# Kernel tuning notes

Measured on AMD Instinct MI355X. Metric: run time of the kernel, lower is better.

## Reference

```python
import jax, jax.numpy as jnp
import numpy as np

ORDER = 3  # polynomial filter order


def _sketch_conv(x, A, W, b, coeffs):
    # z = A @ (x W + b); out = sum_d coeffs[d-1] * z**d  (Horner-free power accumulation)
    z = A @ (x @ W + b)            # [N, out_c]
    p = z
    acc = coeffs[0] * z
    for d in range(1, ORDER):      # small fixed loop over polynomial order
        p = p * z
        acc = acc + coeffs[d] * p
    return acc


def setup_inputs() -> dict:
    key = jax.random.key(0)
    ks = jax.random.split(key, 12)
    N, C_IN, C_H, C_OUT = 8192, 128, 64, 40
    nf_mats = jax.random.normal(ks[0], (N, C_IN), dtype=jnp.float32)
    # scale by 1/sqrt(N) so polynomial powers stay O(1)
    conv_mats = jax.random.normal(ks[1], (N, N), dtype=jnp.float32) / np.float32(np.sqrt(N))
    def lin(k, fi, fo):
        kw, kb = jax.random.split(k)
        W = jax.random.normal(kw, (fi, fo), dtype=jnp.float32) / np.float32(np.sqrt(fi))
        b = jax.random.normal(kb, (fo,), dtype=jnp.float32) * np.float32(0.01)
        return W, b
    W1, b1 = lin(ks[2], C_IN, C_H)
    W2, b2 = lin(ks[3], C_H, C_H)
    W3, b3 = lin(ks[4], C_H, C_OUT)
    base = jnp.array([1.0, 0.0, 0.0], dtype=jnp.float32)
    c1 = base + jax.random.normal(ks[5], (ORDER,), dtype=jnp.float32) * 0.05
    c2 = base + jax.random.normal(ks[6], (ORDER,), dtype=jnp.float32) * 0.05
    c3 = base + jax.random.normal(ks[7], (ORDER,), dtype=jnp.float32) * 0.05
    return {"nf_mats": nf_mats, "conv_mats": conv_mats,
            "W1": W1, "b1": b1, "c1": c1,
            "W2": W2, "b2": b2, "c2": c2,
            "W3": W3, "b3": b3, "c3": c3}


def reference(nf_mats, conv_mats, W1, b1, c1, W2, b2, c2, W3, b3, c3):
    # SketchGCN eval-mode forward: batchnorm=False, dropout inactive.
    x = _sketch_conv(nf_mats, conv_mats, W1, b1, c1)      # first layer
    x = x + _sketch_conv(x, conv_mats, W2, b2, c2)        # residual middle layer
    return _sketch_conv(x, conv_mats, W3, b3, c3)         # output layer
```

## Files before the change

### kernel.cpp

```cpp
#include <hip/hip_runtime.h>
#include <stdint.h>

typedef __bf16 bf16x8 __attribute__((ext_vector_type(8)));
typedef float f32x4 __attribute__((ext_vector_type(4)));

using gvoid = const __attribute__((address_space(1))) void;
using lvoid = __attribute__((address_space(3))) void;

__device__ __forceinline__ unsigned short f2bf(float f) {
    union { float f; unsigned u; } x; x.f = f;
    unsigned u = x.u;
    u += 0x7FFFu + ((u >> 16) & 1u);
    return (unsigned short)(u >> 16);
}
__device__ __forceinline__ unsigned pack2(float lo, float hi) {
    return ((unsigned)f2bf(hi) << 16) | (unsigned)f2bf(lo);
}

template <int CIN>
__global__ __launch_bounds__(256) void small_gemm(const float* __restrict__ X,
                                                  const float* __restrict__ W,
                                                  const float* __restrict__ b,
                                                  int cout,
                                                  unsigned short* __restrict__ Yt) {
    __shared__ float Xs[32 * (CIN + 1)];
    __shared__ float Ws[CIN * 64];
    __shared__ float bs[64];
    const int t = threadIdx.x;
    const int i0 = blockIdx.x * 32;

    for (int e = t; e < 32 * CIN; e += 256) {
        int r = e / CIN, c = e % CIN;
        Xs[r * (CIN + 1) + c] = X[(size_t)(i0 + r) * CIN + c];
    }
    for (int e = t; e < CIN * 64; e += 256) {
        int k = e >> 6, j = e & 63;
        Ws[e] = (j < cout) ? W[k * cout + j] : 0.0f;
    }
    if (t < 64) bs[t] = (t < cout) ? b[t] : 0.0f;
    __syncthreads();

    const int i = t & 31;
    const int jg = t >> 5;
    float acc[8];
#pragma unroll
    for (int jj = 0; jj < 8; ++jj) acc[jj] = 0.0f;

    for (int k = 0; k < CIN; ++k) {
        float xv = Xs[i * (CIN + 1) + k];
        const float4* wr = (const float4*)&Ws[k * 64 + jg * 8];
        float4 w0 = wr[0], w1 = wr[1];
        acc[0] += xv * w0.x; acc[1] += xv * w0.y;
        acc[2] += xv * w0.z; acc[3] += xv * w0.w;
        acc[4] += xv * w1.x; acc[5] += xv * w1.y;
        acc[6] += xv * w1.z; acc[7] += xv * w1.w;
    }
#pragma unroll
    for (int jj = 0; jj < 8; ++jj) {
        int j = jg * 8 + jj;
        Yt[(size_t)j * 8192 + i0 + i] = f2bf(acc[jj] + bs[j]);
    }
}

template <int CONV>
__global__ __launch_bounds__(256, CONV ? 3 : 4)
void big_gemm(const float* __restrict__ Afp,
              unsigned short* __restrict__ Ab,
              const unsigned short* __restrict__ Yt,
              float* __restrict__ P) {
    __shared__ unsigned short As[2][64 * 64];
    __shared__ unsigned short Bs[2][64 * 64];
    const int t = threadIdx.x;
    const int lane = t & 63, wid = t >> 6;
    const int lane15 = lane & 15, lane4 = lane >> 4;
    const int wm = wid >> 1, wn = wid & 1;
    const int row0 = blockIdx.x * 64;
    const int kbase = blockIdx.y * 1024;

    f32x4 acc[2][2];
    const f32x4 z4 = {0.f, 0.f, 0.f, 0.f};
#pragma unroll
    for (int m = 0; m < 2; ++m)
#pragma unroll
        for (int n = 0; n < 2; ++n) acc[m][n] = z4;

    float4 ra[2][2];

    auto loadA_regs = [&](int kt) {
#pragma unroll
        for (int ii = 0; ii < 2; ++ii) {
            int p = ii * 256 + t;
            int r = p >> 3, cl = p & 7;
            const float* gp = Afp + (size_t)(row0 + r) * 8192 + kt + cl * 8;
            ra[ii][0] = *(const float4*)gp;
            ra[ii][1] = *(const float4*)(gp + 4);
        }
    };
    auto writeA = [&](int nb, int kt) {
#pragma unroll
        for (int ii = 0; ii < 2; ++ii) {
            int p = ii * 256 + t;
            int r = p >> 3, cl = p & 7;
            uint4 ch;
            ch.x = pack2(ra[ii][0].x, ra[ii][0].y);
            ch.y = pack2(ra[ii][0].z, ra[ii][0].w);
            ch.z = pack2(ra[ii][1].x, ra[ii][1].y);
            ch.w = pack2(ra[ii][1].z, ra[ii][1].w);
            *(uint4*)&As[nb][((r << 3) | (cl ^ (r & 7))) << 3] = ch;
            *(uint4*)&Ab[(size_t)(row0 + r) * 8192 + kt + cl * 8] = ch;
        }
    };
    auto stageA = [&](int nb, int kt) {
#pragma unroll
        for (int ii = 0; ii < 2; ++ii) {
            int p = ii * 256 + wid * 64 + lane;
            int r = p >> 3;
            int c = (p & 7) ^ (r & 7);
            const unsigned short* gp = Ab + (size_t)(row0 + r) * 8192 + (kt + c * 8);
            unsigned short* lp = &As[nb][(ii * 256 + wid * 64) * 8];
            __builtin_amdgcn_global_load_lds((gvoid*)gp, (lvoid*)lp, 16, 0, 0);
        }
    };
    auto stageB = [&](int nb, int kt) {
#pragma unroll
        for (int ii = 0; ii < 2; ++ii) {
            int q = ii * 256 + wid * 64 + lane;
            int n = q >> 3;
            int c = (q & 7) ^ (n & 7);
            const unsigned short* gp = Yt + (size_t)n * 8192 + (kt + c * 8);
            unsigned short* lp = &Bs[nb][(ii * 256 + wid * 64) * 8];
            __builtin_amdgcn_global_load_lds((gvoid*)gp, (lvoid*)lp, 16, 0, 0);
        }
    };

    if (CONV) {
        loadA_regs(kbase);
        stageB(0, kbase);
        writeA(0, kbase);
    } else {
        stageA(0, kbase);
        stageB(0, kbase);
    }
    __syncthreads();

    int buf = 0;
    const int NIT = 16;
    for (int tt = 0; tt < NIT; ++tt) {
        const bool pre = (tt + 1 < NIT);
        const int kt1 = kbase + (tt + 1) * 64;
        if (pre) {
            if (CONV) {
                loadA_regs(kt1);
                stageB(buf ^ 1, kt1);
            } else {
                stageA(buf ^ 1, kt1);
                stageB(buf ^ 1, kt1);
            }
        }
#pragma unroll
        for (int ks = 0; ks < 2; ++ks) {
            bf16x8 af[2], bfr[2];
#pragma unroll
            for (int m = 0; m < 2; ++m) {
                int r = wm * 32 + m * 16 + lane15;
                int c = ks * 4 + lane4;
                af[m] = *(const bf16x8*)&As[buf][((r << 3) | (c ^ (r & 7))) << 3];
            }
#pragma unroll
            for (int n = 0; n < 2; ++n) {
                int rn = wn * 32 + n * 16 + lane15;
                int c = ks * 4 + lane4;
                bfr[n] = *(const bf16x8*)&Bs[buf][((rn << 3) | (c ^ (rn & 7))) << 3];
            }
#pragma unroll
            for (int m = 0; m < 2; ++m)
#pragma unroll
                for (int n = 0; n < 2; ++n)
                    acc[m][n] = __builtin_amdgcn_mfma_f32_16x16x32_bf16(
                        af[m], bfr[n], acc[m][n], 0, 0, 0);
        }
        if (CONV && pre) writeA(buf ^ 1, kt1);
        __syncthreads();
        buf ^= 1;
    }

    float* Po = P + (size_t)blockIdx.y * (8192 * 64);
#pragma unroll
    for (int m = 0; m < 2; ++m) {
        int r = row0 + wm * 32 + m * 16 + lane4 * 4;
#pragma unroll
        for (int n = 0; n < 2; ++n) {
            int cc = wn * 32 + n * 16 + lane15;
#pragma unroll
            for (int q = 0; q < 4; ++q)
                Po[(size_t)(r + q) * 64 + cc] = acc[m][n][q];
        }
    }
}

template <int MODE>
__global__ __launch_bounds__(256) void fused_reduce(const float* __restrict__ P,
                                                    const float* __restrict__ cf,
                                                    const float* __restrict__ Wn,
                                                    const float* __restrict__ bn,
                                                    int cout,
                                                    float* __restrict__ X1,
                                                    unsigned short* __restrict__ Yt) {
    __shared__ float Xs[64 * 33];
    __shared__ float Ws[64 * 64];
    __shared__ float bs[64];
    const int t = threadIdx.x;
    const int i0 = blockIdx.x * 32;
    const int NT4 = 8192 * 64 / 4;
    const float4* P4 = (const float4*)P;
    float4* X14 = (float4*)X1;

    for (int e = t; e < 64 * 64; e += 256) {
        int k = e >> 6, j = e & 63;
        Ws[e] = (j < cout) ? Wn[k * cout + j] : 0.0f;
    }
    if (t < 64) bs[t] = (t < cout) ? bn[t] : 0.0f;
    const float c0 = cf[0], c1 = cf[1], c2 = cf[2];

#pragma unroll
    for (int s = 0; s < 2; ++s) {
        int e4 = s * 256 + t;
        int i = e4 >> 4, jc = e4 & 15;
        int base4 = (i0 + i) * 16 + jc;
        float4 z = {0.f, 0.f, 0.f, 0.f};
#pragma unroll
        for (int ks = 0; ks < 8; ++ks) {
            float4 p = P4[(size_t)ks * NT4 + base4];
            z.x += p.x; z.y += p.y; z.z += p.z; z.w += p.w;
        }
        float4 v;
        v.x = z.x * (c0 + z.x * (c1 + z.x * c2));
        v.y = z.y * (c0 + z.y * (c1 + z.y * c2));
        v.z = z.z * (c0 + z.z * (c1 + z.z * c2));
        v.w = z.w * (c0 + z.w * (c1 + z.w * c2));
        if (MODE == 0) {
            X14[base4] = v;
        } else {
            float4 xr = X14[base4];
            v.x += xr.x; v.y += xr.y; v.z += xr.z; v.w += xr.w;
        }
        Xs[(jc * 4 + 0) * 33 + i] = v.x;
        Xs[(jc * 4 + 1) * 33 + i] = v.y;
        Xs[(jc * 4 + 2) * 33 + i] = v.z;
        Xs[(jc * 4 + 3) * 33 + i] = v.w;
    }
    __syncthreads();

    const int i = t & 31;
    const int jg = t >> 5;
    float acc[8];
#pragma unroll
    for (int jj = 0; jj < 8; ++jj) acc[jj] = 0.0f;
    for (int k = 0; k < 64; ++k) {
        float xv = Xs[k * 33 + i];
        const float4* wr = (const float4*)&Ws[k * 64 + jg * 8];
        float4 w0 = wr[0], w1 = wr[1];
        acc[0] += xv * w0.x; acc[1] += xv * w0.y;
        acc[2] += xv * w0.z; acc[3] += xv * w0.w;
        acc[4] += xv * w1.x; acc[5] += xv * w1.y;
        acc[6] += xv * w1.z; acc[7] += xv * w1.w;
    }
#pragma unroll
    for (int jj = 0; jj < 8; ++jj) {
        int j = jg * 8 + jj;
        Yt[(size_t)j * 8192 + i0 + i] = f2bf(acc[jj] + bs[j]);
    }
}

__global__ void reduce_out(const float* __restrict__ P, const float* __restrict__ cf,
                           float* __restrict__ out) {
    int e4 = blockIdx.x * 256 + threadIdx.x;
    const int NT4 = 8192 * 64 / 4;
    const float4* P4 = (const float4*)P;
    float4 z = {0.f, 0.f, 0.f, 0.f};
#pragma unroll
    for (int ks = 0; ks < 8; ++ks) {
        float4 p = P4[(size_t)ks * NT4 + e4];
        z.x += p.x; z.y += p.y; z.z += p.z; z.w += p.w;
    }
    float c0 = cf[0], c1 = cf[1], c2 = cf[2];
    float4 v;
    v.x = z.x * (c0 + z.x * (c1 + z.x * c2));
    v.y = z.y * (c0 + z.y * (c1 + z.y * c2));
    v.z = z.z * (c0 + z.z * (c1 + z.z * c2));
    v.w = z.w * (c0 + z.w * (c1 + z.w * c2));
    int i = e4 >> 4, jc = e4 & 15;
    if (jc < 10) ((float4*)out)[i * 10 + jc] = v;
}

extern "C" void kernel_launch(void* const* d_in, const int* in_sizes, int n_in,
                              void* d_out, int out_size, void* d_ws, size_t ws_size,
                              hipStream_t stream) {
    const float* nf   = (const float*)d_in[0];
    const float* Amat = (const float*)d_in[1];
    const float* W1   = (const float*)d_in[2];
    const float* b1   = (const float*)d_in[3];
    const float* c1   = (const float*)d_in[4];
    const float* W2   = (const float*)d_in[5];
    const float* b2   = (const float*)d_in[6];
    const float* c2   = (const float*)d_in[7];
    const float* W3   = (const float*)d_in[8];
    const float* b3   = (const float*)d_in[9];
    const float* c3   = (const float*)d_in[10];
    float* out = (float*)d_out;

    char* ws = (char*)d_ws;
    unsigned short* Abf = (unsigned short*)(ws);
    unsigned short* Yt  = (unsigned short*)(ws + 134217728);
    float* X1           = (float*)(ws + 135266304);
    float* Pp           = (float*)(ws + 137363456);

    small_gemm<128><<<256, 256, 0, stream>>>(nf, W1, b1, 64, Yt);
    big_gemm<1><<<dim3(128, 8), 256, 0, stream>>>(Amat, Abf, Yt, Pp);
    fused_reduce<0><<<256, 256, 0, stream>>>(Pp, c1, W2, b2, 64, X1, Yt);

    big_gemm<0><<<dim3(128, 8), 256, 0, stream>>>(nullptr, Abf, Yt, Pp);
    fused_reduce<1><<<256, 256, 0, stream>>>(Pp, c2, W3, b3, 40, X1, Yt);

    big_gemm<0><<<dim3(128, 8), 256, 0, stream>>>(nullptr, Abf, Yt, Pp);
    reduce_out<<<512, 256, 0, stream>>>(Pp, c3, out);
}
```

Baseline: 223.4 us.

## Load GEMM fragments directly from global into registers, drop LDS staging

The big GEMM kernel no longer stages A and B tiles through shared memory with barriers. Each lane now loads its MFMA fragments straight from global memory into registers, double-buffered in registers across k-steps. In the conversion pass, only one of the two waves sharing a row writes the bf16 A cache. This removes LDS traffic and __syncthreads, but each A and B tile is now fetched by two waves, doubling global/L2 reads, and the row-strided per-lane 16-byte loads coalesce less well.

```diff
diff --git a/kernel.cpp b/kernel.cpp
--- a/kernel.cpp
+++ b/kernel.cpp
@@ -3,9 +3,6 @@
 
 typedef __bf16 bf16x8 __attribute__((ext_vector_type(8)));
 typedef float f32x4 __attribute__((ext_vector_type(4)));
-
-using gvoid = const __attribute__((address_space(1))) void;
-using lvoid = __attribute__((address_space(3))) void;
 
 __device__ __forceinline__ unsigned short f2bf(float f) {
     union { float f; unsigned u; } x; x.f = f;
@@ -16,6 +13,7 @@
 __device__ __forceinline__ unsigned pack2(float lo, float hi) {
     return ((unsigned)f2bf(hi) << 16) | (unsigned)f2bf(lo);
 }
+union U16 { uint4 u; bf16x8 v; };
 
 template <int CIN>
 __global__ __launch_bounds__(256) void small_gemm(const float* __restrict__ X,
@@ -68,14 +66,15 @@
               unsigned short* __restrict__ Ab,
               const unsigned short* __restrict__ Yt,
               float* __restrict__ P) {
-    __shared__ unsigned short As[2][64 * 64];
-    __shared__ unsigned short Bs[2][64 * 64];
     const int t = threadIdx.x;
     const int lane = t & 63, wid = t >> 6;
     const int lane15 = lane & 15, lane4 = lane >> 4;
     const int wm = wid >> 1, wn = wid & 1;
     const int row0 = blockIdx.x * 64;
     const int kbase = blockIdx.y * 1024;
+    const int arow = row0 + wm * 32 + lane15;
+    const int brow = wn * 32 + lane15;
+    const int kc = lane4 * 8;
 
     f32x4 acc[2][2];
     const f32x4 z4 = {0.f, 0.f, 0.f, 0.f};
@@ -84,104 +83,89 @@
 #pragma unroll
         for (int n = 0; n < 2; ++n) acc[m][n] = z4;
 
-    float4 ra[2][2];
-
-    auto loadA_regs = [&](int kt) {
-#pragma unroll
-        for (int ii = 0; ii < 2; ++ii) {
-            int p = ii * 256 + t;
-            int r = p >> 3, cl = p & 7;
-            const float* gp = Afp + (size_t)(row0 + r) * 8192 + kt + cl * 8;
-            ra[ii][0] = *(const float4*)gp;
-            ra[ii][1] = *(const float4*)(gp + 4);
-        }
+    auto loadB = [&](bf16x8 (&bb)[2][2], int kt) {
+#pragma unroll
+        for (int n = 0; n < 2; ++n)
+#pragma unroll
+            for (int ks = 0; ks < 2; ++ks)
+                bb[n][ks] = *(const bf16x8*)(Yt + (size_t)(brow + n * 16) * 8192 +
+                                             kt + ks * 32 + kc);
     };
-    auto writeA = [&](int nb, int kt) {
-#pragma unroll
-        for (int ii = 0; ii < 2; ++ii) {
-            int p = ii * 256 + t;
-            int r = p >> 3, cl = p & 7;
-            uint4 ch;
-            ch.x = pack2(ra[ii][0].x, ra[ii][0].y);
-            ch.y = pack2(ra[ii][0].z, ra[ii][0].w);
-            ch.z = pack2(ra[ii][1].x, ra[ii][1].y);
-            ch.w = pack2(ra[ii][1].z, ra[ii][1].w);
-            *(uint4*)&As[nb][((r << 3) | (cl ^ (r & 7))) << 3] = ch;
-            *(uint4*)&Ab[(size_t)(row0 + r) * 8192 + kt + cl * 8] = ch;
-        }
-    };
-    auto stageA = [&](int nb, int kt) {
-#pragma unroll
-        for (int ii = 0; ii < 2; ++ii) {
-            int p = ii * 256 + wid * 64 + lane;
-            int r = p >> 3;
-            int c = (p & 7) ^ (r & 7);
-            const unsigned short* gp = Ab + (size_t)(row0 + r) * 8192 + (kt + c * 8);
-            unsigned short* lp = &As[nb][(ii * 256 + wid * 64) * 8];
-            __builtin_amdgcn_global_load_lds((gvoid*)gp, (lvoid*)lp, 16, 0, 0);
-        }
-    };
-    auto stageB = [&](int nb, int kt) {
-#pragma unroll
-        for (int ii = 0; ii < 2; ++ii) {
-            int q = ii * 256 + wid * 64 + lane;
-            int n = q >> 3;
-            int c = (q & 7) ^ (n & 7);
-            const unsigned short* gp = Yt + (size_t)n * 8192 + (kt + c * 8);
-            unsigned short* lp = &Bs[nb][(ii * 256 + wid * 64) * 8];
-            __builtin_amdgcn_global_load_lds((gvoid*)gp, (lvoid*)lp, 16, 0, 0);
-        }
-    };
-
-    if (CONV) {
-        loadA_regs(kbase);
-        stageB(0, kbase);
-        writeA(0, kbase);
+
+    if constexpr (CONV) {
+        auto loadT = [&](float4 (&ra)[2][2][2], bf16x8 (&bb)[2][2], int kt) {
+#pragma unroll
+            for (int m = 0; m < 2; ++m)
+#pragma unroll
+                for (int ks = 0; ks < 2; ++ks) {
+                    const float* gp = Afp + (size_t)(arow + m * 16) * 8192 +
+                                      kt + ks * 32 + kc;
+                    ra[m][ks][0] = *(const float4*)gp;
+                    ra[m][ks][1] = *(const float4*)(gp + 4);
+                }
+            loadB(bb, kt);
+        };
+        auto comp = [&](float4 (&ra)[2][2][2], bf16x8 (&bb)[2][2], int kt) {
+#pragma unroll
+            for (int ks = 0; ks < 2; ++ks) {
+                bf16x8 af[2];
+#pragma unroll
+                for (int m = 0; m < 2; ++m) {
+                    U16 u;
+                    u.u.x = pack2(ra[m][ks][0].x, ra[m][ks][0].y);
+                    u.u.y = pack2(ra[m][ks][0].z, ra[m][ks][0].w);
+                    u.u.z = pack2(ra[m][ks][1].x, ra[m][ks][1].y);
+                    u.u.w = pack2(ra[m][ks][1].z, ra[m][ks][1].w);
+                    af[m] = u.v;
+                    if (wn == 0)
+                        *(uint4*)(Ab + (size_t)(arow + m * 16) * 8192 +
+                                  kt + ks * 32 + kc) = u.u;
+                }
+#pragma unroll
+                for (int m = 0; m < 2; ++m)
+#pragma unroll
+                    for (int n = 0; n < 2; ++n)
+                        acc[m][n] = __builtin_amdgcn_mfma_f32_16x16x32_bf16(
+                            af[m], bb[n][ks], acc[m][n], 0, 0, 0);
+            }
+        };
+        float4 raA[2][2][2], raB[2][2][2];
+        bf16x8 bbA[2][2], bbB[2][2];
+        loadT(raA, bbA, kbase);
+        for (int tt = 0; tt < 16; tt += 2) {
+            if (tt + 1 < 16) loadT(raB, bbB, kbase + (tt + 1) * 64);
+            comp(raA, bbA, kbase + tt * 64);
+            if (tt + 2 < 16) loadT(raA, bbA, kbase + (tt + 2) * 64);
+            if (tt + 1 < 16) comp(raB, bbB, kbase + (tt + 1) * 64);
+        }
     } else {
-        stageA(0, kbase);
-        stageB(0, kbase);
-    }
-    __syncthreads();
-
-    int buf = 0;
-    const int NIT = 16;
-    for (int tt = 0; tt < NIT; ++tt) {
-        const bool pre = (tt + 1 < NIT);
-        const int kt1 = kbase + (tt + 1) * 64;
-        if (pre) {
-            if (CONV) {
-                loadA_regs(kt1);
-                stageB(buf ^ 1, kt1);
-            } else {
-                stageA(buf ^ 1, kt1);
-                stageB(buf ^ 1, kt1);
-            }
-        }
-#pragma unroll
-        for (int ks = 0; ks < 2; ++ks) {
-            bf16x8 af[2], bfr[2];
-#pragma unroll
-            for (int m = 0; m < 2; ++m) {
-                int r = wm * 32 + m * 16 + lane15;
-                int c = ks * 4 + lane4;
-                af[m] = *(const bf16x8*)&As[buf][((r << 3) | (c ^ (r & 7))) << 3];
-            }
-#pragma unroll
-            for (int n = 0; n < 2; ++n) {
-                int rn = wn * 32 + n * 16 + lane15;
-                int c = ks * 4 + lane4;
-                bfr[n] = *(const bf16x8*)&Bs[buf][((rn << 3) | (c ^ (rn & 7))) << 3];
-            }
+        auto loadT = [&](bf16x8 (&aa)[2][2], bf16x8 (&bb)[2][2], int kt) {
 #pragma unroll
             for (int m = 0; m < 2; ++m)
 #pragma unroll
-                for (int n = 0; n < 2; ++n)
-                    acc[m][n] = __builtin_amdgcn_mfma_f32_16x16x32_bf16(
-                        af[m], bfr[n], acc[m][n], 0, 0, 0);
-        }
-        if (CONV && pre) writeA(buf ^ 1, kt1);
-        __syncthreads();
-        buf ^= 1;
+                for (int ks = 0; ks < 2; ++ks)
+                    aa[m][ks] = *(const bf16x8*)(Ab + (size_t)(arow + m * 16) * 8192 +
+                                                 kt + ks * 32 + kc);
+            loadB(bb, kt);
+        };
+        auto comp = [&](bf16x8 (&aa)[2][2], bf16x8 (&bb)[2][2]) {
+#pragma unroll
+            for (int ks = 0; ks < 2; ++ks)
+#pragma unroll
+                for (int m = 0; m < 2; ++m)
+#pragma unroll
+                    for (int n = 0; n < 2; ++n)
+                        acc[m][n] = __builtin_amdgcn_mfma_f32_16x16x32_bf16(
+                            aa[m][ks], bb[n][ks], acc[m][n], 0, 0, 0);
+        };
+        bf16x8 aaA[2][2], aaB[2][2], bbA[2][2], bbB[2][2];
+        loadT(aaA, bbA, kbase);
+        for (int tt = 0; tt < 16; tt += 2) {
+            if (tt + 1 < 16) loadT(aaB, bbB, kbase + (tt + 1) * 64);
+            comp(aaA, bbA);
+            if (tt + 2 < 16) loadT(aaA, bbA, kbase + (tt + 2) * 64);
+            if (tt + 1 < 16) comp(aaB, bbB);
+        }
     }
 
     float* Po = P + (size_t)blockIdx.y * (8192 * 64);
```

After: 326.9 us. 1.46x slower.

## Split A bf16 conversion into standalone kernel and use async-load barriers in GEMM

Applied to the files above, without the earlier changes.

Moves the fp32→bf16 conversion of the large conv matrix out of the first big GEMM into a separate streaming conversion kernel, so all three GEMMs share one template that stages A and B straight into LDS with direct global-to-LDS loads. The main loop now waits with explicit vmcnt and s_barrier, so the prefetch of the next tile stays in flight during the current tile's MFMAs. The first GEMM could also run at the higher occupancy bound. In exchange the conversion adds an extra full read of the fp32 matrix and a write of the bf16 copy as its own launch. The hand-written waitcnt counts must match the number of outstanding loads or the kernel will read stale LDS data.

```diff
diff --git a/kernel.cpp b/kernel.cpp
--- a/kernel.cpp
+++ b/kernel.cpp
@@ -15,6 +15,24 @@
 }
 __device__ __forceinline__ unsigned pack2(float lo, float hi) {
     return ((unsigned)f2bf(hi) << 16) | (unsigned)f2bf(lo);
+}
+
+__global__ __launch_bounds__(256) void convert_bf16(const float* __restrict__ in,
+                                                    unsigned short* __restrict__ out,
+                                                    int n8) {
+    int idx = blockIdx.x * 256 + threadIdx.x;
+    int stride = gridDim.x * 256;
+    const float4* in4 = (const float4*)in;
+    uint4* out8 = (uint4*)out;
+    for (int i = idx; i < n8; i += stride) {
+        float4 a = in4[2 * i], b = in4[2 * i + 1];
+        uint4 o;
+        o.x = pack2(a.x, a.y);
+        o.y = pack2(a.z, a.w);
+        o.z = pack2(b.x, b.y);
+        o.w = pack2(b.z, b.w);
+        out8[i] = o;
+    }
 }
 
 template <int CIN>
@@ -62,10 +80,8 @@
     }
 }
 
-template <int CONV>
-__global__ __launch_bounds__(256, CONV ? 3 : 4)
-void big_gemm(const float* __restrict__ Afp,
-              unsigned short* __restrict__ Ab,
+__global__ __launch_bounds__(256, 4)
+void big_gemm(const unsigned short* __restrict__ Ab,
               const unsigned short* __restrict__ Yt,
               float* __restrict__ P) {
     __shared__ unsigned short As[2][64 * 64];
@@ -84,33 +100,7 @@
 #pragma unroll
         for (int n = 0; n < 2; ++n) acc[m][n] = z4;
 
-    float4 ra[2][2];
-
-    auto loadA_regs = [&](int kt) {
-#pragma unroll
-        for (int ii = 0; ii < 2; ++ii) {
-            int p = ii * 256 + t;
-            int r = p >> 3, cl = p & 7;
-            const float* gp = Afp + (size_t)(row0 + r) * 8192 + kt + cl * 8;
-            ra[ii][0] = *(const float4*)gp;
-            ra[ii][1] = *(const float4*)(gp + 4);
-        }
-    };
-    auto writeA = [&](int nb, int kt) {
-#pragma unroll
-        for (int ii = 0; ii < 2; ++ii) {
-            int p = ii * 256 + t;
-            int r = p >> 3, cl = p & 7;
-            uint4 ch;
-            ch.x = pack2(ra[ii][0].x, ra[ii][0].y);
-            ch.y = pack2(ra[ii][0].z, ra[ii][0].w);
-            ch.z = pack2(ra[ii][1].x, ra[ii][1].y);
-            ch.w = pack2(ra[ii][1].z, ra[ii][1].w);
-            *(uint4*)&As[nb][((r << 3) | (cl ^ (r & 7))) << 3] = ch;
-            *(uint4*)&Ab[(size_t)(row0 + r) * 8192 + kt + cl * 8] = ch;
-        }
-    };
-    auto stageA = [&](int nb, int kt) {
+    auto stage = [&](int nb, int kt) {
 #pragma unroll
         for (int ii = 0; ii < 2; ++ii) {
             int p = ii * 256 + wid * 64 + lane;
@@ -120,8 +110,6 @@
             unsigned short* lp = &As[nb][(ii * 256 + wid * 64) * 8];
             __builtin_amdgcn_global_load_lds((gvoid*)gp, (lvoid*)lp, 16, 0, 0);
         }
-    };
-    auto stageB = [&](int nb, int kt) {
 #pragma unroll
         for (int ii = 0; ii < 2; ++ii) {
             int q = ii * 256 + wid * 64 + lane;
@@ -133,29 +121,14 @@
         }
     };
 
-    if (CONV) {
-        loadA_regs(kbase);
-        stageB(0, kbase);
-        writeA(0, kbase);
-    } else {
-        stageA(0, kbase);
-        stageB(0, kbase);
-    }
-    __syncthreads();
-
+    stage(0, kbase);
     int buf = 0;
-    const int NIT = 16;
-    for (int tt = 0; tt < NIT; ++tt) {
-        const bool pre = (tt + 1 < NIT);
-        const int kt1 = kbase + (tt + 1) * 64;
-        if (pre) {
-            if (CONV) {
-                loadA_regs(kt1);
-                stageB(buf ^ 1, kt1);
-            } else {
-                stageA(buf ^ 1, kt1);
-                stageB(buf ^ 1, kt1);
-            }
+    for (int tt = 0; tt < 16; ++tt) {
+        if (tt + 1 < 16) {
+            stage(buf ^ 1, kbase + (tt + 1) * 64);
+            asm volatile("s_waitcnt vmcnt(4)\n\ts_barrier" ::: "memory");
+        } else {
+            asm volatile("s_waitcnt vmcnt(0)\n\ts_barrier" ::: "memory");
         }
 #pragma unroll
         for (int ks = 0; ks < 2; ++ks) {
@@ -179,8 +152,7 @@
                     acc[m][n] = __builtin_amdgcn_mfma_f32_16x16x32_bf16(
                         af[m], bfr[n], acc[m][n], 0, 0, 0);
         }
-        if (CONV && pre) writeA(buf ^ 1, kt1);
-        __syncthreads();
+        asm volatile("s_barrier" ::: "memory");
         buf ^= 1;
     }
 
@@ -315,13 +287,15 @@
     float* X1           = (float*)(ws + 135266304);
     float* Pp           = (float*)(ws + 137363456);
 
+    convert_bf16<<<2048, 256, 0, stream>>>(Amat, Abf, 8192 * 8192 / 8);
     small_gemm<128><<<256, 256, 0, stream>>>(nf, W1, b1, 64, Yt);
-    big_gemm<1><<<dim3(128, 8), 256, 0, stream>>>(Amat, Abf, Yt, Pp);
+
+    big_gemm<<<dim3(128, 8), 256, 0, stream>>>(Abf, Yt, Pp);
     fused_reduce<0><<<256, 256, 0, stream>>>(Pp, c1, W2, b2, 64, X1, Yt);
 
-    big_gemm<0><<<dim3(128, 8), 256, 0, stream>>>(nullptr, Abf, Yt, Pp);
+    big_gemm<<<dim3(128, 8), 256, 0, stream>>>(Abf, Yt, Pp);
     fused_reduce<1><<<256, 256, 0, stream>>>(Pp, c2, W3, b3, 40, X1, Yt);
 
-    big_gemm<0><<<dim3(128, 8), 256, 0, stream>>>(nullptr, Abf, Yt, Pp);
+    big_gemm<<<dim3(128, 8), 256, 0, stream>>>(Abf, Yt, Pp);
     reduce_out<<<512, 256, 0, stream>>>(Pp, c3, out);
 }
```

After: 204.0 us. 8.7% less time.
